# Kernel optimization log

Measured on AMD Instinct MI355X. Metric: run time of the kernel, lower is better.

## Reference

```python
import jax, jax.numpy as jnp
import numpy as np

B, C, H, W = 4, 256, 128, 128
RATION = 1
Cr = C // RATION


def conv1x1(x, Wt, b):
    # pointwise conv: [B,C,H,W] x [O,C] -> [B,O,H,W]
    return jnp.einsum('bchw,oc->bohw', x, Wt) + b[None, :, None, None]


def setup_inputs() -> dict:
    key = jax.random.key(0)
    ks = jax.random.split(key, 10)
    s_in = 1.0 / np.sqrt(C)
    s_up = 1.0 / np.sqrt(Cr)
    return {
        'x': jax.random.normal(ks[0], (B, C, H, W), dtype=jnp.float32),
        'Wq': jax.random.normal(ks[1], (Cr, C), dtype=jnp.float32) * s_in,
        'bq': jax.random.normal(ks[2], (Cr,), dtype=jnp.float32) * s_in,
        'Wk': jax.random.normal(ks[3], (Cr, C), dtype=jnp.float32) * s_in,
        'bk': jax.random.normal(ks[4], (Cr,), dtype=jnp.float32) * s_in,
        'Wv': jax.random.normal(ks[5], (Cr, C), dtype=jnp.float32) * s_in,
        'bv': jax.random.normal(ks[6], (Cr,), dtype=jnp.float32) * s_in,
        'Wu': jax.random.normal(ks[7], (C, Cr), dtype=jnp.float32) * s_up,
        'bu': jax.random.normal(ks[8], (C,), dtype=jnp.float32) * s_up,
        'gamma': jax.random.normal(ks[9], (1,), dtype=jnp.float32) * 0.1,
    }


def reference(x, Wq, bq, Wk, bk, Wv, bv, Wu, bu, gamma):
    b, c, h, w = x.shape
    # Q/K/V: relu(1x1 conv), then raw contiguous reshape [B,Cr,H,W] -> [B,W,Cr*H]
    x_Qw = jax.nn.relu(conv1x1(x, Wq, bq)).reshape(b, w, -1)              # [B, W, Cr*H]
    x_Kw = jnp.swapaxes(jax.nn.relu(conv1x1(x, Wk, bk)).reshape(b, w, -1), 1, 2)  # [B, Cr*H, W]
    x_Vw = jnp.swapaxes(jax.nn.relu(conv1x1(x, Wv, bv)).reshape(b, w, -1), 1, 2)  # [B, Cr*H, W]
    # attention over Width axis; softmax over dim=1 as in the original
    attn = jax.nn.softmax(jnp.matmul(x_Qw, x_Kw), axis=1)                 # [B, W, W]
    out1 = jnp.matmul(x_Vw, attn)                                         # [B, Cr*H, W]
    out = out1.reshape(b, c // RATION, h, w) * gamma
    out_w = conv1x1(out, Wu, bu)                                          # [B, C, H, W]
    return (out_w, x_Qw, x_Kw, x_Vw, gamma, attn)
```

## Files before the change

kernel.cpp:

```cpp
#include <hip/hip_runtime.h>
#include <hip/hip_bf16.h>


typedef __attribute__((ext_vector_type(8))) short bf16x8;
typedef __attribute__((ext_vector_type(4))) float f4;

#define MFMA16(a, b, c) __builtin_amdgcn_mfma_f32_16x16x32_bf16(a, b, c, 0, 0, 0)

__device__ __forceinline__ unsigned short f2bf(float f) {
  union { float f; unsigned u; } v; v.f = f;
  unsigned r = v.u + 0x7fffu + ((v.u >> 16) & 1u);
  return (unsigned short)(r >> 16);
}
__device__ __forceinline__ float bf2f(unsigned short h) {
  union { unsigned u; float f; } v; v.u = ((unsigned)h) << 16;
  return v.f;
}
__device__ __forceinline__ void splitf(float f, unsigned short &hi, unsigned short &lo) {
  unsigned short h = f2bf(f);
  hi = h; lo = f2bf(f - bf2f(h));
}

__device__ __forceinline__ void split8t(float4 a, float4 b, bf16x8 &hi, bf16x8 &lo) {
  union { bf16x8 v; unsigned u[4]; } uh, ul;
  const unsigned* ua = (const unsigned*)&a;
  const unsigned* ub = (const unsigned*)&b;
  const float* fa = (const float*)&a;
  const float* fb = (const float*)&b;
#pragma unroll
  for (int e = 0; e < 2; ++e) {
    uh.u[e]     = __builtin_amdgcn_perm(ua[2*e+1], ua[2*e], 0x07060302u);
    uh.u[2 + e] = __builtin_amdgcn_perm(ub[2*e+1], ub[2*e], 0x07060302u);
    union { float f; unsigned u; } p0, p1, q0, q1;
    p0.u = ua[2*e] & 0xffff0000u;   p1.u = ua[2*e+1] & 0xffff0000u;
    p0.f = fa[2*e] - p0.f;          p1.f = fa[2*e+1] - p1.f;
    ul.u[e] = __builtin_amdgcn_perm(p1.u, p0.u, 0x07060302u);
    q0.u = ub[2*e] & 0xffff0000u;   q1.u = ub[2*e+1] & 0xffff0000u;
    q0.f = fb[2*e] - q0.f;          q1.f = fb[2*e+1] - q1.f;
    ul.u[2 + e] = __builtin_amdgcn_perm(q1.u, q0.u, 0x07060302u);
  }
  hi = uh.v; lo = ul.v;
}

__device__ __forceinline__ bf16x8 pack8t(float4 a, float4 b) {
  union { bf16x8 v; unsigned u[4]; } r;
  const unsigned* ua = (const unsigned*)&a;
  const unsigned* ub = (const unsigned*)&b;
  r.u[0] = __builtin_amdgcn_perm(ua[1], ua[0], 0x07060302u);
  r.u[1] = __builtin_amdgcn_perm(ua[3], ua[2], 0x07060302u);
  r.u[2] = __builtin_amdgcn_perm(ub[1], ub[0], 0x07060302u);
  r.u[3] = __builtin_amdgcn_perm(ub[3], ub[2], 0x07060302u);
  return r.v;
}

__global__ __launch_bounds__(256) void k_prep(
    const float* __restrict__ Wq, const float* __restrict__ Wk,
    const float* __restrict__ Wv, const float* __restrict__ Wu,
    unsigned short* __restrict__ wqh, unsigned short* __restrict__ wql,
    unsigned short* __restrict__ wkh, unsigned short* __restrict__ wkl,
    unsigned short* __restrict__ wvh, unsigned short* __restrict__ wuh) {
  const int i = blockIdx.x * 256 + threadIdx.x;
  unsigned short h, lo2;
  splitf(Wq[i], h, lo2); wqh[i] = h; wql[i] = lo2;
  splitf(Wk[i], h, lo2); wkh[i] = h; wkl[i] = lo2;
  wvh[i] = f2bf(Wv[i]);
  wuh[i] = f2bf(Wu[i]);
}

__global__ __launch_bounds__(256) void k_qkv(
    const float* __restrict__ x,
    const unsigned short* __restrict__ wqh, const unsigned short* __restrict__ wql,
    const unsigned short* __restrict__ wkh, const unsigned short* __restrict__ wkl,
    const unsigned short* __restrict__ wvh,
    const float* __restrict__ bq, const float* __restrict__ bk,
    const float* __restrict__ bv,
    float* __restrict__ outQ, float* __restrict__ outKT, float* __restrict__ outVT,
    float* __restrict__ K2f, float* __restrict__ Sbuf) {
  const int pb = blockIdx.x, b = blockIdx.y;
  const int p0 = pb * 64;
  const int t = threadIdx.x;

  if (pb == 0)
    for (int i = t; i < 16384; i += 256) Sbuf[b * 16384 + i] = 0.0f;

  __shared__ unsigned short xthi[64][264];
  __shared__ unsigned short xtlo[64][264];
  __shared__ float tbuf[64][132];

  {
    const int cp = t & 127;
    const int ph = (t >> 7) * 32;
    const float* r0 = x + ((size_t)b * 256 + 2 * cp) * 16384 + p0 + ph;
    const float* r1 = r0 + 16384;
#pragma unroll
    for (int q = 0; q < 8; ++q) {
      float4 v0 = *(const float4*)(r0 + 4 * q);
      float4 v1 = *(const float4*)(r1 + 4 * q);
      const unsigned* u0 = (const unsigned*)&v0;
      const unsigned* u1 = (const unsigned*)&v1;
      const float* f0 = (const float*)&v0;
      const float* f1 = (const float*)&v1;
#pragma unroll
      for (int e = 0; e < 4; ++e) {
        const int p = ph + 4 * q + e;
        *(unsigned*)&xthi[p][2 * cp] = __builtin_amdgcn_perm(u1[e], u0[e], 0x07060302u);
        union { float f; unsigned u; } l0, l1;
        l0.u = u0[e] & 0xffff0000u;  l1.u = u1[e] & 0xffff0000u;
        l0.f = f0[e] - l0.f;         l1.f = f1[e] - l1.f;
        *(unsigned*)&xtlo[p][2 * cp] = __builtin_amdgcn_perm(l1.u, l0.u, 0x07060302u);
      }
    }
  }
  __syncthreads();

  const int wv = t >> 6, l = t & 63;
  const int lr = l & 15, lkq = l >> 4, lk = lkq * 8;
  const size_t ob = (size_t)b * 4194304;
  const f4 fz = {0.f, 0.f, 0.f, 0.f};
  f4 acc[4][4];

#define CONV_PASS(WHI, WLO, SPLIT)                                        \
  {                                                                       \
    _Pragma("unroll") for (int mt = 0; mt < 4; ++mt)                      \
    _Pragma("unroll") for (int nt = 0; nt < 4; ++nt) acc[mt][nt] = fz;    \
    _Pragma("unroll 1") for (int kk = 0; kk < 8; ++kk) {                  \
      const int c0 = kk * 32 + lk;                                        \
      bf16x8 ahi[4], alo[4], bhi[4], blo[4];                              \
      _Pragma("unroll") for (int mt = 0; mt < 4; ++mt) {                  \
        const int o = wv * 64 + mt * 16 + lr;                             \
        ahi[mt] = *(const bf16x8*)(WHI + o * 256 + c0);                   \
        if (SPLIT) alo[mt] = *(const bf16x8*)(WLO + o * 256 + c0);        \
      }                                                                   \
      _Pragma("unroll") for (int nt = 0; nt < 4; ++nt) {                  \
        bhi[nt] = *(const bf16x8*)&xthi[nt * 16 + lr][c0];                \
        if (SPLIT) blo[nt] = *(const bf16x8*)&xtlo[nt * 16 + lr][c0];     \
      }                                                                   \
      _Pragma("unroll") for (int mt = 0; mt < 4; ++mt)                    \
      _Pragma("unroll") for (int nt = 0; nt < 4; ++nt) {                  \
        acc[mt][nt] = MFMA16(ahi[mt], bhi[nt], acc[mt][nt]);              \
        if (SPLIT) {                                                      \
          acc[mt][nt] = MFMA16(ahi[mt], blo[nt], acc[mt][nt]);            \
          acc[mt][nt] = MFMA16(alo[mt], bhi[nt], acc[mt][nt]);            \
        }                                                                 \
      }                                                                   \
    }                                                                     \
  }

#define TRANSPOSE_OUT(DST)                                                   \
  _Pragma("unroll") for (int par = 0; par < 2; ++par) {                      \
    __syncthreads();                                                         \
    const int ibase = wv * 32 + lkq * 2;                                     \
    _Pragma("unroll") for (int mt = 0; mt < 4; ++mt)                         \
    _Pragma("unroll") for (int m = 0; m < 2; ++m) {                          \
      const int i = ibase + mt * 8 + m;                                      \
      const int e = par + 2 * m;       \
      _Pragma("unroll") for (int nt = 0; nt < 4; ++nt)                       \
        tbuf[nt * 16 + lr][i] = acc[mt][nt][e];                              \
    }                                                                        \
    __syncthreads();                                                         \
    {                                                                        \
      const int pr = t >> 2, seg = (t & 3) * 32;                             \
      float* dst = DST + ob + (size_t)(par * 16384 + p0 + pr) * 128 + seg;   \
      _Pragma("unroll") for (int q2 = 0; q2 < 8; ++q2)                       \
        *(float4*)(dst + 4 * q2) = *(const float4*)&tbuf[pr][seg + 4 * q2];  \
    }                                                                        \
  }

  CONV_PASS(wqh, wql, 1)
  {
    const int rbase = wv * 64 + lkq * 4;
#pragma unroll
    for (int mt = 0; mt < 4; ++mt)
#pragma unroll
      for (int e = 0; e < 4; ++e) {
        const int o = rbase + mt * 16 + e;
        const float bb = bq[o];
#pragma unroll
        for (int nt = 0; nt < 4; ++nt)
          outQ[ob + (size_t)o * 16384 + (p0 + nt * 16 + lr)] =
              fmaxf(acc[mt][nt][e] + bb, 0.0f);
      }
  }

  CONV_PASS(wkh, wkl, 1)
  {
    const int rbase = wv * 64 + lkq * 4;
#pragma unroll
    for (int mt = 0; mt < 4; ++mt)
#pragma unroll
      for (int e = 0; e < 4; ++e) {
        const int o = rbase + mt * 16 + e;
        const float bb = bk[o];
#pragma unroll
        for (int nt = 0; nt < 4; ++nt) {
          const float v = fmaxf(acc[mt][nt][e] + bb, 0.0f);
          acc[mt][nt][e] = v;
          K2f[ob + (size_t)o * 16384 + (p0 + nt * 16 + lr)] = v;
        }
      }
  }
  TRANSPOSE_OUT(outKT)

  CONV_PASS(wvh, wvh, 0)
  {
    const int rbase = wv * 64 + lkq * 4;
#pragma unroll
    for (int mt = 0; mt < 4; ++mt)
#pragma unroll
      for (int e = 0; e < 4; ++e) {
        const int o = rbase + mt * 16 + e;
        const float bb = bv[o];
#pragma unroll
        for (int nt = 0; nt < 4; ++nt)
          acc[mt][nt][e] = fmaxf(acc[mt][nt][e] + bb, 0.0f);
      }
  }
  TRANSPOSE_OUT(outVT)
#undef CONV_PASS
#undef TRANSPOSE_OUT
}

__global__ __launch_bounds__(256) void k_qk(
    const float* __restrict__ Q2, const float* __restrict__ K2f,
    float* __restrict__ Sbuf) {
  const int s = blockIdx.x, b = blockIdx.y;
  const int t = threadIdx.x;
  const int wvv = t >> 6, l = t & 63;
  const int wm = (wvv >> 1) * 64, wn = (wvv & 1) * 64;
  const int lr = l & 15, lkq = l >> 4, lk = lkq * 8;
  const size_t qb = (size_t)b * 4194304;
  const int jb = s * 1024;
  const f4 fz = {0.f, 0.f, 0.f, 0.f};
  f4 acc[4][4];
#pragma unroll
  for (int mt = 0; mt < 4; ++mt)
#pragma unroll
    for (int nt = 0; nt < 4; ++nt) acc[mt][nt] = fz;

#pragma unroll 1
  for (int kk = 0; kk < 32; ++kk) {
    const int j = jb + kk * 32 + lk;
    bf16x8 ahi[4], alo[4], bhi[4], blo[4];
#pragma unroll
    for (int mt = 0; mt < 4; ++mt) {
      const float* r = Q2 + qb + (size_t)(wm + mt * 16 + lr) * 32768 + j;
      split8t(*(const float4*)r, *(const float4*)(r + 4), ahi[mt], alo[mt]);
    }
#pragma unroll
    for (int nt = 0; nt < 4; ++nt) {
      const float* r = K2f + qb + (size_t)(wn + nt * 16 + lr) * 32768 + j;
      split8t(*(const float4*)r, *(const float4*)(r + 4), bhi[nt], blo[nt]);
    }
#pragma unroll
    for (int mt = 0; mt < 4; ++mt)
#pragma unroll
      for (int nt = 0; nt < 4; ++nt) {
        acc[mt][nt] = MFMA16(ahi[mt], bhi[nt], acc[mt][nt]);
        acc[mt][nt] = MFMA16(ahi[mt], blo[nt], acc[mt][nt]);
        acc[mt][nt] = MFMA16(alo[mt], bhi[nt], acc[mt][nt]);
      }
  }
#pragma unroll
  for (int mt = 0; mt < 4; ++mt)
#pragma unroll
    for (int e = 0; e < 4; ++e) {
      const int i1 = wm + mt * 16 + lkq * 4 + e;
#pragma unroll
      for (int nt = 0; nt < 4; ++nt) {
        const int i2 = wn + nt * 16 + lr;
        atomicAdd(&Sbuf[b * 16384 + i1 * 128 + i2], acc[mt][nt][e]);
      }
    }
}

__global__ __launch_bounds__(256) void k_softmax(
    const float* __restrict__ Sbuf, const float* __restrict__ gin,
    float* __restrict__ attnO, float* __restrict__ gammaO,
    unsigned short* __restrict__ attnTg) {
  const int ch = blockIdx.x, b = blockIdx.y;
  const int t = threadIdx.x;
  const int col = t & 31, part = t >> 5;
  const int cbase = ch * 32;
  __shared__ float sc[128][33];
  __shared__ float redA[8][33];
  __shared__ float redB[8][33];
#pragma unroll
  for (int rr = 0; rr < 16; ++rr) {
    const int i1 = part * 16 + rr;
    sc[i1][col] = Sbuf[b * 16384 + i1 * 128 + cbase + col];
  }
  __syncthreads();
  float mx = -3.4e38f;
#pragma unroll
  for (int rr = 0; rr < 16; ++rr) mx = fmaxf(mx, sc[part * 16 + rr][col]);
  redA[part][col] = mx;
  __syncthreads();
  if (part == 0) {
    float m2 = redA[0][col];
#pragma unroll
    for (int pp = 1; pp < 8; ++pp) m2 = fmaxf(m2, redA[pp][col]);
    redA[0][col] = m2;
  }
  __syncthreads();
  const float m = redA[0][col];
  float sum = 0.f;
#pragma unroll
  for (int rr = 0; rr < 16; ++rr) {
    const int i1 = part * 16 + rr;
    const float e = expf(sc[i1][col] - m);
    sc[i1][col] = e;
    sum += e;
  }
  redB[part][col] = sum;
  __syncthreads();
  if (part == 0) {
    float s2 = 0.f;
#pragma unroll
    for (int pp = 0; pp < 8; ++pp) s2 += redB[pp][col];
    redB[0][col] = 1.0f / s2;
  }
  __syncthreads();
  const float inv = redB[0][col];
  const float g = gin[0];
#pragma unroll
  for (int rr = 0; rr < 16; ++rr) {
    const int i1 = part * 16 + rr;
    const float v = sc[i1][col] * inv;
    attnO[b * 16384 + i1 * 128 + cbase + col] = v;
    attnTg[(size_t)b * 16384 + (size_t)(cbase + col) * 128 + i1] = f2bf(v * g);
  }
  if (b == 0 && ch == 0 && t == 0) gammaO[0] = gin[0];
}

__global__ __launch_bounds__(256) void k_pv(
    const float* __restrict__ VT, const unsigned short* __restrict__ attnTg,
    unsigned short* __restrict__ outb) {
  const int jblk = blockIdx.x, b = blockIdx.y;
  const int t = threadIdx.x;
  const int wvv = t >> 6, l = t & 63;
  const int lr = l & 15, lkq = l >> 4, lk = lkq * 8;
  const size_t vb = (size_t)b * 4194304;
  const int j0 = jblk * 256 + wvv * 64;
  const f4 fz = {0.f, 0.f, 0.f, 0.f};
  f4 acc[4][8];
#pragma unroll
  for (int mt = 0; mt < 4; ++mt)
#pragma unroll
    for (int nt = 0; nt < 8; ++nt) acc[mt][nt] = fz;

#pragma unroll
  for (int kk = 0; kk < 4; ++kk) {
    const int k0 = kk * 32 + lk;
    bf16x8 av[4], bt[8];
#pragma unroll
    for (int mt = 0; mt < 4; ++mt) {
      const float* r = VT + vb + (size_t)(j0 + mt * 16 + lr) * 128 + k0;
      av[mt] = pack8t(*(const float4*)r, *(const float4*)(r + 4));
    }
#pragma unroll
    for (int nt = 0; nt < 8; ++nt)
      bt[nt] = *(const bf16x8*)(attnTg + (size_t)b * 16384 +
                                (size_t)(nt * 16 + lr) * 128 + k0);
#pragma unroll
    for (int mt = 0; mt < 4; ++mt)
#pragma unroll
      for (int nt = 0; nt < 8; ++nt)
        acc[mt][nt] = MFMA16(av[mt], bt[nt], acc[mt][nt]);
  }
#pragma unroll
  for (int mt = 0; mt < 4; ++mt)
#pragma unroll
    for (int e = 0; e < 4; ++e) {
      const int j = j0 + mt * 16 + lkq * 4 + e;
#pragma unroll
      for (int nt = 0; nt < 8; ++nt)
        outb[vb + (size_t)j * 128 + (nt * 16 + lr)] = f2bf(acc[mt][nt][e]);
    }
}

__global__ __launch_bounds__(256) void k_up(
    const unsigned short* __restrict__ outb, const unsigned short* __restrict__ wuh,
    const float* __restrict__ bu, float* __restrict__ outw) {
  const int pb = blockIdx.x, b = blockIdx.y;
  const int p0 = pb * 64;
  const int t = threadIdx.x;
  __shared__ unsigned short ot[64][264];
  {
    const int cp = t & 127;
    const int ph = (t >> 7) * 32;
    const unsigned short* row0 = outb + ((size_t)b * 256 + 2 * cp) * 16384 + p0 + ph;
    const unsigned* r0 = (const unsigned*)row0;
    const unsigned* r1 = (const unsigned*)(row0 + 16384);
#pragma unroll
    for (int k = 0; k < 16; ++k) {
      const unsigned a0 = r0[k], a1 = r1[k];
      const int p = ph + 2 * k;
      *(unsigned*)&ot[p][2 * cp] = (a0 & 0xffffu) | (a1 << 16);
      *(unsigned*)&ot[p + 1][2 * cp] = (a0 >> 16) | (a1 & 0xffff0000u);
    }
  }
  __syncthreads();
  const int wv = t >> 6, l = t & 63;
  const int lr = l & 15, lkq = l >> 4, lk = lkq * 8;
  const f4 fz = {0.f, 0.f, 0.f, 0.f};
  f4 acc[4][4];
#pragma unroll
  for (int mt = 0; mt < 4; ++mt)
#pragma unroll
    for (int nt = 0; nt < 4; ++nt) acc[mt][nt] = fz;

#pragma unroll 1
  for (int kk = 0; kk < 8; ++kk) {
    const int c0 = kk * 32 + lk;
    bf16x8 a[4], bt[4];
#pragma unroll
    for (int mt = 0; mt < 4; ++mt)
      a[mt] = *(const bf16x8*)(wuh + (wv * 64 + mt * 16 + lr) * 256 + c0);
#pragma unroll
    for (int nt = 0; nt < 4; ++nt)
      bt[nt] = *(const bf16x8*)&ot[nt * 16 + lr][c0];
#pragma unroll
    for (int mt = 0; mt < 4; ++mt)
#pragma unroll
      for (int nt = 0; nt < 4; ++nt)
        acc[mt][nt] = MFMA16(a[mt], bt[nt], acc[mt][nt]);
  }
  const size_t ob2 = (size_t)b * 4194304;
  const int rbase = wv * 64 + lkq * 4;
#pragma unroll
  for (int mt = 0; mt < 4; ++mt)
#pragma unroll
    for (int e = 0; e < 4; ++e) {
      const int o = rbase + mt * 16 + e;
      const float bb = bu[o];
#pragma unroll
      for (int nt = 0; nt < 4; ++nt)
        outw[ob2 + (size_t)o * 16384 + (p0 + nt * 16 + lr)] = acc[mt][nt][e] + bb;
    }
}

extern "C" void kernel_launch(void* const* d_in, const int* in_sizes, int n_in,
                              void* d_out, int out_size, void* d_ws, size_t ws_size,
                              hipStream_t stream) {
  (void)in_sizes; (void)n_in; (void)out_size; (void)ws_size;
  const float* x  = (const float*)d_in[0];
  const float* Wq = (const float*)d_in[1];
  const float* bq = (const float*)d_in[2];
  const float* Wk = (const float*)d_in[3];
  const float* bk = (const float*)d_in[4];
  const float* Wv = (const float*)d_in[5];
  const float* bv = (const float*)d_in[6];
  const float* Wu = (const float*)d_in[7];
  const float* bu = (const float*)d_in[8];
  const float* gm = (const float*)d_in[9];

  float* dout   = (float*)d_out;
  float* outw   = dout;
  float* outQ   = dout + 16777216;
  float* outKT  = dout + 33554432;
  float* outVT  = dout + 50331648;
  float* gammaO = dout + 67108864;
  float* attnO  = dout + 67108865;

  char* wsb = (char*)d_ws;
  float* K2f   = (float*)(wsb);
  float* Sbuf  = (float*)(wsb + 67108864);
  unsigned short* attnTg = (unsigned short*)(wsb + 67371008);
  unsigned short* outb   = (unsigned short*)(wsb + 67502080);
  unsigned short* wqh = (unsigned short*)(wsb + 101056512);
  unsigned short* wql = wqh + 65536;
  unsigned short* wkh = wql + 65536;
  unsigned short* wkl = wkh + 65536;
  unsigned short* wvh = wkl + 65536;
  unsigned short* wuh = wvh + 65536;

  k_prep<<<dim3(256), dim3(256), 0, stream>>>(Wq, Wk, Wv, Wu,
                                              wqh, wql, wkh, wkl, wvh, wuh);
  k_qkv<<<dim3(256, 4), dim3(256), 0, stream>>>(x, wqh, wql, wkh, wkl, wvh,
                                                bq, bk, bv,
                                                outQ, outKT, outVT, K2f, Sbuf);
  k_qk<<<dim3(32, 4), dim3(256), 0, stream>>>(outQ, K2f, Sbuf);
  k_softmax<<<dim3(4, 4), dim3(256), 0, stream>>>(Sbuf, gm, attnO, gammaO, attnTg);
  k_pv<<<dim3(128, 4), dim3(256), 0, stream>>>(outVT, attnTg, outb);
  k_up<<<dim3(256, 4), dim3(256), 0, stream>>>(outb, wuh, bu, outw);
}
```

Baseline: 616.2 us.

## Split QK into partial-sum slabs with separate reduction, shrink QKV tiles, shuffle softmax

The QKV conv kernel now uses 32-pixel tiles with twice as many blocks and a smaller shared footprint, reusing the lo buffer as the transpose scratch. The QK^T kernel drops the float atomics into one zeroed buffer. It now has 128 slabs per batch, each writing a private partial score matrix, followed by a new deterministic reduction kernel. Softmax is rewritten to use warp shuffles over more blocks instead of shared-memory reductions. The changes aim to raise occupancy and parallelism and remove atomic contention, at the cost of an extra kernel and about 32 MB of partial-sum traffic.

```diff
diff --git a/kernel.cpp b/kernel.cpp
--- a/kernel.cpp
+++ b/kernel.cpp
@@ -67,7 +67,7 @@
   wuh[i] = f2bf(Wu[i]);
 }
 
-__global__ __launch_bounds__(256) void k_qkv(
+__global__ __launch_bounds__(256, 4) void k_qkv(
     const float* __restrict__ x,
     const unsigned short* __restrict__ wqh, const unsigned short* __restrict__ wql,
     const unsigned short* __restrict__ wkh, const unsigned short* __restrict__ wkl,
@@ -75,25 +75,22 @@
     const float* __restrict__ bq, const float* __restrict__ bk,
     const float* __restrict__ bv,
     float* __restrict__ outQ, float* __restrict__ outKT, float* __restrict__ outVT,
-    float* __restrict__ K2f, float* __restrict__ Sbuf) {
+    float* __restrict__ K2f) {
   const int pb = blockIdx.x, b = blockIdx.y;
-  const int p0 = pb * 64;
+  const int p0 = pb * 32;
   const int t = threadIdx.x;
 
-  if (pb == 0)
-    for (int i = t; i < 16384; i += 256) Sbuf[b * 16384 + i] = 0.0f;
-
-  __shared__ unsigned short xthi[64][264];
-  __shared__ unsigned short xtlo[64][264];
-  __shared__ float tbuf[64][132];
+  __shared__ __align__(16) unsigned short xthi[32][264];
+  __shared__ __align__(16) unsigned short xtlo[32][264];
+  float (*tbuf)[132] = reinterpret_cast<float (*)[132]>(&xtlo[0][0]);
 
   {
     const int cp = t & 127;
-    const int ph = (t >> 7) * 32;
-    const float* r0 = x + ((size_t)b * 256 + 2 * cp) * 16384 + p0 + ph;
+    const int hh = (t >> 7) * 16;
+    const float* r0 = x + ((size_t)b * 256 + 2 * cp) * 16384 + p0 + hh;
     const float* r1 = r0 + 16384;
 #pragma unroll
-    for (int q = 0; q < 8; ++q) {
+    for (int q = 0; q < 4; ++q) {
       float4 v0 = *(const float4*)(r0 + 4 * q);
       float4 v1 = *(const float4*)(r1 + 4 * q);
       const unsigned* u0 = (const unsigned*)&v0;
@@ -102,7 +99,7 @@
       const float* f1 = (const float*)&v1;
 #pragma unroll
       for (int e = 0; e < 4; ++e) {
-        const int p = ph + 4 * q + e;
+        const int p = hh + 4 * q + e;
         *(unsigned*)&xthi[p][2 * cp] = __builtin_amdgcn_perm(u1[e], u0[e], 0x07060302u);
         union { float f; unsigned u; } l0, l1;
         l0.u = u0[e] & 0xffff0000u;  l1.u = u1[e] & 0xffff0000u;
@@ -117,26 +114,26 @@
   const int lr = l & 15, lkq = l >> 4, lk = lkq * 8;
   const size_t ob = (size_t)b * 4194304;
   const f4 fz = {0.f, 0.f, 0.f, 0.f};
-  f4 acc[4][4];
+  f4 acc[4][2];
 
 #define CONV_PASS(WHI, WLO, SPLIT)                                        \
   {                                                                       \
     _Pragma("unroll") for (int mt = 0; mt < 4; ++mt)                      \
-    _Pragma("unroll") for (int nt = 0; nt < 4; ++nt) acc[mt][nt] = fz;    \
+    _Pragma("unroll") for (int nt = 0; nt < 2; ++nt) acc[mt][nt] = fz;    \
     _Pragma("unroll 1") for (int kk = 0; kk < 8; ++kk) {                  \
       const int c0 = kk * 32 + lk;                                        \
-      bf16x8 ahi[4], alo[4], bhi[4], blo[4];                              \
+      bf16x8 ahi[4], alo[4], bhi[2], blo[2];                              \
       _Pragma("unroll") for (int mt = 0; mt < 4; ++mt) {                  \
         const int o = wv * 64 + mt * 16 + lr;                             \
         ahi[mt] = *(const bf16x8*)(WHI + o * 256 + c0);                   \
         if (SPLIT) alo[mt] = *(const bf16x8*)(WLO + o * 256 + c0);        \
       }                                                                   \
-      _Pragma("unroll") for (int nt = 0; nt < 4; ++nt) {                  \
+      _Pragma("unroll") for (int nt = 0; nt < 2; ++nt) {                  \
         bhi[nt] = *(const bf16x8*)&xthi[nt * 16 + lr][c0];                \
         if (SPLIT) blo[nt] = *(const bf16x8*)&xtlo[nt * 16 + lr][c0];     \
       }                                                                   \
       _Pragma("unroll") for (int mt = 0; mt < 4; ++mt)                    \
-      _Pragma("unroll") for (int nt = 0; nt < 4; ++nt) {                  \
+      _Pragma("unroll") for (int nt = 0; nt < 2; ++nt) {                  \
         acc[mt][nt] = MFMA16(ahi[mt], bhi[nt], acc[mt][nt]);              \
         if (SPLIT) {                                                      \
           acc[mt][nt] = MFMA16(ahi[mt], blo[nt], acc[mt][nt]);            \
@@ -149,20 +146,19 @@
 #define TRANSPOSE_OUT(DST)                                                   \
   _Pragma("unroll") for (int par = 0; par < 2; ++par) {                      \
     __syncthreads();                                                         \
-    const int ibase = wv * 32 + lkq * 2;                                     \
     _Pragma("unroll") for (int mt = 0; mt < 4; ++mt)                         \
     _Pragma("unroll") for (int m = 0; m < 2; ++m) {                          \
-      const int i = ibase + mt * 8 + m;                                      \
+      const int i = wv * 32 + mt * 8 + lkq * 2 + m;                          \
       const int e = par + 2 * m;       \
-      _Pragma("unroll") for (int nt = 0; nt < 4; ++nt)                       \
+      _Pragma("unroll") for (int nt = 0; nt < 2; ++nt)                       \
         tbuf[nt * 16 + lr][i] = acc[mt][nt][e];                              \
     }                                                                        \
     __syncthreads();                                                         \
     {                                                                        \
-      const int pr = t >> 2, seg = (t & 3) * 32;                             \
-      float* dst = DST + ob + (size_t)(par * 16384 + p0 + pr) * 128 + seg;   \
-      _Pragma("unroll") for (int q2 = 0; q2 < 8; ++q2)                       \
-        *(float4*)(dst + 4 * q2) = *(const float4*)&tbuf[pr][seg + 4 * q2];  \
+      const int pr = t >> 3, c4 = (t & 7) * 16;                              \
+      float* dst = DST + ob + (size_t)(par * 16384 + p0 + pr) * 128 + c4;    \
+      _Pragma("unroll") for (int q2 = 0; q2 < 4; ++q2)                       \
+        *(float4*)(dst + 4 * q2) = *(const float4*)&tbuf[pr][c4 + 4 * q2];   \
     }                                                                        \
   }
 
@@ -176,7 +172,7 @@
         const int o = rbase + mt * 16 + e;
         const float bb = bq[o];
 #pragma unroll
-        for (int nt = 0; nt < 4; ++nt)
+        for (int nt = 0; nt < 2; ++nt)
           outQ[ob + (size_t)o * 16384 + (p0 + nt * 16 + lr)] =
               fmaxf(acc[mt][nt][e] + bb, 0.0f);
       }
@@ -192,7 +188,7 @@
         const int o = rbase + mt * 16 + e;
         const float bb = bk[o];
 #pragma unroll
-        for (int nt = 0; nt < 4; ++nt) {
+        for (int nt = 0; nt < 2; ++nt) {
           const float v = fmaxf(acc[mt][nt][e] + bb, 0.0f);
           acc[mt][nt][e] = v;
           K2f[ob + (size_t)o * 16384 + (p0 + nt * 16 + lr)] = v;
@@ -211,7 +207,7 @@
         const int o = rbase + mt * 16 + e;
         const float bb = bv[o];
 #pragma unroll
-        for (int nt = 0; nt < 4; ++nt)
+        for (int nt = 0; nt < 2; ++nt)
           acc[mt][nt][e] = fmaxf(acc[mt][nt][e] + bb, 0.0f);
       }
   }
@@ -220,116 +216,103 @@
 #undef TRANSPOSE_OUT
 }
 
-__global__ __launch_bounds__(256) void k_qk(
+__global__ __launch_bounds__(512, 4) void k_qk(
     const float* __restrict__ Q2, const float* __restrict__ K2f,
-    float* __restrict__ Sbuf) {
+    float* __restrict__ Spart) {
   const int s = blockIdx.x, b = blockIdx.y;
   const int t = threadIdx.x;
   const int wvv = t >> 6, l = t & 63;
-  const int wm = (wvv >> 1) * 64, wn = (wvv & 1) * 64;
+  const int wm = (wvv >> 2) * 64, wn = (wvv & 3) * 32;
   const int lr = l & 15, lkq = l >> 4, lk = lkq * 8;
   const size_t qb = (size_t)b * 4194304;
-  const int jb = s * 1024;
+  const int jb = s * 256;
   const f4 fz = {0.f, 0.f, 0.f, 0.f};
-  f4 acc[4][4];
-#pragma unroll
-  for (int mt = 0; mt < 4; ++mt)
-#pragma unroll
-    for (int nt = 0; nt < 4; ++nt) acc[mt][nt] = fz;
+  f4 acc[4][2];
+#pragma unroll
+  for (int mt = 0; mt < 4; ++mt)
+#pragma unroll
+    for (int nt = 0; nt < 2; ++nt) acc[mt][nt] = fz;
 
 #pragma unroll 1
-  for (int kk = 0; kk < 32; ++kk) {
+  for (int kk = 0; kk < 8; ++kk) {
     const int j = jb + kk * 32 + lk;
-    bf16x8 ahi[4], alo[4], bhi[4], blo[4];
+    bf16x8 ahi[4], alo[4], bhi[2], blo[2];
 #pragma unroll
     for (int mt = 0; mt < 4; ++mt) {
       const float* r = Q2 + qb + (size_t)(wm + mt * 16 + lr) * 32768 + j;
       split8t(*(const float4*)r, *(const float4*)(r + 4), ahi[mt], alo[mt]);
     }
 #pragma unroll
-    for (int nt = 0; nt < 4; ++nt) {
+    for (int nt = 0; nt < 2; ++nt) {
       const float* r = K2f + qb + (size_t)(wn + nt * 16 + lr) * 32768 + j;
       split8t(*(const float4*)r, *(const float4*)(r + 4), bhi[nt], blo[nt]);
     }
 #pragma unroll
     for (int mt = 0; mt < 4; ++mt)
 #pragma unroll
-      for (int nt = 0; nt < 4; ++nt) {
+      for (int nt = 0; nt < 2; ++nt) {
         acc[mt][nt] = MFMA16(ahi[mt], bhi[nt], acc[mt][nt]);
         acc[mt][nt] = MFMA16(ahi[mt], blo[nt], acc[mt][nt]);
         acc[mt][nt] = MFMA16(alo[mt], bhi[nt], acc[mt][nt]);
       }
   }
+  float* out = Spart + ((size_t)(b * 128 + s)) * 16384;
 #pragma unroll
   for (int mt = 0; mt < 4; ++mt)
 #pragma unroll
     for (int e = 0; e < 4; ++e) {
       const int i1 = wm + mt * 16 + lkq * 4 + e;
 #pragma unroll
-      for (int nt = 0; nt < 4; ++nt) {
-        const int i2 = wn + nt * 16 + lr;
-        atomicAdd(&Sbuf[b * 16384 + i1 * 128 + i2], acc[mt][nt][e]);
-      }
-    }
+      for (int nt = 0; nt < 2; ++nt)
+        out[i1 * 128 + (wn + nt * 16 + lr)] = acc[mt][nt][e];
+    }
+}
+
+__global__ __launch_bounds__(256) void k_sred(
+    const float* __restrict__ Spart, float* __restrict__ S) {
+  const int e = blockIdx.x * 256 + threadIdx.x;
+  const int b = blockIdx.y;
+  const float* p = Spart + (size_t)b * 128 * 16384 + e;
+  float s0 = 0.f, s1 = 0.f, s2 = 0.f, s3 = 0.f;
+#pragma unroll 4
+  for (int s = 0; s < 128; s += 4) {
+    s0 += p[(size_t)s * 16384];
+    s1 += p[(size_t)(s + 1) * 16384];
+    s2 += p[(size_t)(s + 2) * 16384];
+    s3 += p[(size_t)(s + 3) * 16384];
+  }
+  S[b * 16384 + e] = (s0 + s1) + (s2 + s3);
 }
 
 __global__ __launch_bounds__(256) void k_softmax(
-    const float* __restrict__ Sbuf, const float* __restrict__ gin,
+    const float* __restrict__ S, const float* __restrict__ gin,
     float* __restrict__ attnO, float* __restrict__ gammaO,
     unsigned short* __restrict__ attnTg) {
-  const int ch = blockIdx.x, b = blockIdx.y;
+  const int cb = blockIdx.x, b = blockIdx.y;
   const int t = threadIdx.x;
-  const int col = t & 31, part = t >> 5;
-  const int cbase = ch * 32;
-  __shared__ float sc[128][33];
-  __shared__ float redA[8][33];
-  __shared__ float redB[8][33];
-#pragma unroll
-  for (int rr = 0; rr < 16; ++rr) {
-    const int i1 = part * 16 + rr;
-    sc[i1][col] = Sbuf[b * 16384 + i1 * 128 + cbase + col];
-  }
-  __syncthreads();
-  float mx = -3.4e38f;
-#pragma unroll
-  for (int rr = 0; rr < 16; ++rr) mx = fmaxf(mx, sc[part * 16 + rr][col]);
-  redA[part][col] = mx;
-  __syncthreads();
-  if (part == 0) {
-    float m2 = redA[0][col];
-#pragma unroll
-    for (int pp = 1; pp < 8; ++pp) m2 = fmaxf(m2, redA[pp][col]);
-    redA[0][col] = m2;
-  }
-  __syncthreads();
-  const float m = redA[0][col];
+  const int col = cb * 8 + (t >> 5);
+  const int r = t & 31;
+  const float* Sb = S + b * 16384;
+  float v[4];
+#pragma unroll
+  for (int j = 0; j < 4; ++j) v[j] = Sb[(r + 32 * j) * 128 + col];
+  float m = fmaxf(fmaxf(v[0], v[1]), fmaxf(v[2], v[3]));
+#pragma unroll
+  for (int k = 16; k >= 1; k >>= 1) m = fmaxf(m, __shfl_xor(m, k, 32));
   float sum = 0.f;
 #pragma unroll
-  for (int rr = 0; rr < 16; ++rr) {
-    const int i1 = part * 16 + rr;
-    const float e = expf(sc[i1][col] - m);
-    sc[i1][col] = e;
-    sum += e;
-  }
-  redB[part][col] = sum;
-  __syncthreads();
-  if (part == 0) {
-    float s2 = 0.f;
-#pragma unroll
-    for (int pp = 0; pp < 8; ++pp) s2 += redB[pp][col];
-    redB[0][col] = 1.0f / s2;
-  }
-  __syncthreads();
-  const float inv = redB[0][col];
+  for (int j = 0; j < 4; ++j) { v[j] = expf(v[j] - m); sum += v[j]; }
+#pragma unroll
+  for (int k = 16; k >= 1; k >>= 1) sum += __shfl_xor(sum, k, 32);
+  const float inv = 1.0f / sum;
   const float g = gin[0];
 #pragma unroll
-  for (int rr = 0; rr < 16; ++rr) {
-    const int i1 = part * 16 + rr;
-    const float v = sc[i1][col] * inv;
-    attnO[b * 16384 + i1 * 128 + cbase + col] = v;
-    attnTg[(size_t)b * 16384 + (size_t)(cbase + col) * 128 + i1] = f2bf(v * g);
-  }
-  if (b == 0 && ch == 0 && t == 0) gammaO[0] = gin[0];
+  for (int j = 0; j < 4; ++j) {
+    const float p2 = v[j] * inv;
+    attnO[b * 16384 + (r + 32 * j) * 128 + col] = p2;
+    attnTg[(size_t)b * 16384 + (size_t)col * 128 + (r + 32 * j)] = f2bf(p2 * g);
+  }
+  if (b == 0 && cb == 0 && t == 0) gammaO[0] = gin[0];
 }
 
 __global__ __launch_bounds__(256) void k_pv(
@@ -464,9 +447,10 @@
 
   char* wsb = (char*)d_ws;
   float* K2f   = (float*)(wsb);
-  float* Sbuf  = (float*)(wsb + 67108864);
-  unsigned short* attnTg = (unsigned short*)(wsb + 67371008);
-  unsigned short* outb   = (unsigned short*)(wsb + 67502080);
+  float* Spart = (float*)(wsb + 67108864);
+  unsigned short* outb = (unsigned short*)(wsb + 67108864);
+  float* S     = (float*)(wsb + 100663296);
+  unsigned short* attnTg = (unsigned short*)(wsb + 100925440);
   unsigned short* wqh = (unsigned short*)(wsb + 101056512);
   unsigned short* wql = wqh + 65536;
   unsigned short* wkh = wql + 65536;
@@ -476,11 +460,12 @@
 
   k_prep<<<dim3(256), dim3(256), 0, stream>>>(Wq, Wk, Wv, Wu,
                                               wqh, wql, wkh, wkl, wvh, wuh);
-  k_qkv<<<dim3(256, 4), dim3(256), 0, stream>>>(x, wqh, wql, wkh, wkl, wvh,
+  k_qkv<<<dim3(512, 4), dim3(256), 0, stream>>>(x, wqh, wql, wkh, wkl, wvh,
                                                 bq, bk, bv,
-                                                outQ, outKT, outVT, K2f, Sbuf);
-  k_qk<<<dim3(32, 4), dim3(256), 0, stream>>>(outQ, K2f, Sbuf);
-  k_softmax<<<dim3(4, 4), dim3(256), 0, stream>>>(Sbuf, gm, attnO, gammaO, attnTg);
+                                                outQ, outKT, outVT, K2f);
+  k_qk<<<dim3(128, 4), dim3(512), 0, stream>>>(outQ, K2f, Spart);
+  k_sred<<<dim3(64, 4), dim3(256), 0, stream>>>(Spart, S);
+  k_softmax<<<dim3(16, 4), dim3(256), 0, stream>>>(S, gm, attnO, gammaO, attnTg);
   k_pv<<<dim3(128, 4), dim3(256), 0, stream>>>(outVT, attnTg, outb);
   k_up<<<dim3(256, 4), dim3(256), 0, stream>>>(outb, wuh, bu, outw);
 }
```

After: 591.5 us. 4.0% less time.
